# Kernel tuning notes

Hardware: AMD Instinct MI355X
Metric: run time of the kernel (lower is better)

The kernel has to match this reference:

```python
import jax, jax.numpy as jnp
import numpy as np

B, T, N, C = 2, 8, 10242, 64
K, NBR, O = 9, 7, 64


def setup_inputs() -> dict:
    key = jax.random.key(0)
    k1, k2, k3, k4, k5 = jax.random.split(key, 5)
    x = jax.random.normal(k1, (B, T, N, C), dtype=jnp.float32)
    index = jax.random.randint(k2, (N, NBR), 0, N, dtype=jnp.int64)
    itp_mat = jax.random.uniform(k3, (N, NBR, K), dtype=jnp.float32)
    conv_w = jax.random.normal(k4, (O, C, 1, K), dtype=jnp.float32) * (1.0 / np.sqrt(C * K))
    conv_b = jax.random.normal(k5, (O,), dtype=jnp.float32) * 0.01
    return {"x": x, "index": index, "itp_mat": itp_mat, "conv_w": conv_w, "conv_b": conv_b}


def reference(x, index, itp_mat, conv_w, conv_b):
    b, t, n, c = x.shape
    o = conv_w.shape[0]
    # (B,T,N,C) -> (B*T, C, N)
    feats = x.reshape(b * t, n, c).transpose(0, 2, 1)
    # gather neighbors: (BT, C, N, NBR)
    nb = feats[:, :, index]
    # per-node interpolation matmul: (BT, C, N, K)
    itp = jnp.einsum('bcnj,njk->bcnk', nb, itp_mat)
    # Conv2d with kernel (1,K) on width K collapses K fully: (BT, O, N)
    out = jnp.einsum('bcnk,ock->bon', itp, conv_w[:, :, 0, :]) + conv_b[None, :, None]
    # (B, T, O, N) -> (B, T, N, O)
    return out.reshape(b, t, o, n).transpose(0, 1, 3, 2)
```

## Files before the change

kernel.cpp:

```cpp
#include <hip/hip_runtime.h>

#define BT    16
#define NN    10242
#define CC    64
#define KK    9
#define NBR_  7
#define OO    64
#define CK    576
#define MT    16
#define RS    584
#define KT    18

using frag  = __attribute__((ext_vector_type(8))) short;
using f32x4 = __attribute__((ext_vector_type(4))) float;

static __device__ __forceinline__ unsigned short f2bf(float f) {
    union { float f; unsigned u; } v; v.f = f;
    unsigned r = v.u + 0x7fffu + ((v.u >> 16) & 1u);
    return (unsigned short)(r >> 16);
}

static __device__ __forceinline__ unsigned pk2(float a, float b) {
    unsigned r;
    asm("v_cvt_pk_bf16_f32 %0, %1, %2" : "=v"(r) : "v"(a), "v"(b));
    return r;
}

__global__ void pack_w_kernel(const float* __restrict__ w, unsigned short* __restrict__ wb) {
    int i = blockIdx.x * blockDim.x + threadIdx.x;
    if (i >= KT * 4 * 64 * 8) return;
    int j  = i & 7;
    int l  = (i >> 3) & 63;
    int ct = (i >> 9) & 3;
    int t  = i >> 11;
    int q  = t * 32 + (l >> 4) * 8 + j;
    int o  = ct * 16 + (l & 15);
    int c, k;
    if (q < 512) { c = (q & 255) >> 2; k = (q >> 8) * 4 + (q & 3); }
    else         { c = q - 512;        k = 8; }
    wb[i] = f2bf(w[(o * CC + c) * KK + k]);
}

__global__ __launch_bounds__(256, 8) void sphere_conv_kernel(
    const float* __restrict__ x,
    const int*   __restrict__ index,
    const float* __restrict__ m,
    const unsigned short* __restrict__ wb,
    const float* __restrict__ bias,
    float*       __restrict__ out)
{
    __shared__ unsigned short itp_s[MT * RS];

    const int tid  = threadIdx.x;
    const int nt   = blockIdx.x;
    const int bt   = blockIdx.y;
    const int n0   = nt * MT;
    const int w    = tid >> 6;
    const int lane = tid & 63;

    {
        const float* xbt = x + (size_t)bt * NN * CC;

        int nu[4];
        #pragma unroll
        for (int r = 0; r < 4; ++r) {
            const int n = n0 + w * 4 + r;
            nu[r] = __builtin_amdgcn_readfirstlane(n < NN ? n : (NN - 1));
        }

        float xv[4][NBR_];
        #pragma unroll
        for (int r = 0; r < 4; ++r) {
            const int* ip = index + nu[r] * NBR_;
            #pragma unroll
            for (int j = 0; j < NBR_; ++j)
                xv[r][j] = xbt[(size_t)ip[j] * CC + lane];
        }
        __builtin_amdgcn_sched_barrier(0);

        #pragma unroll
        for (int r = 0; r < 4; ++r) {
            const int ns = w * 4 + r;
            const float* mp = m + nu[r] * (NBR_ * KK);
            float acc[KK];
            #pragma unroll
            for (int k = 0; k < KK; ++k) acc[k] = 0.f;
            #pragma unroll
            for (int j = 0; j < NBR_; ++j)
                #pragma unroll
                for (int k = 0; k < KK; ++k)
                    acc[k] = fmaf(xv[r][j], mp[j * KK + k], acc[k]);

            uint2 q0, q1;
            q0.x = pk2(acc[0], acc[1]);
            q0.y = pk2(acc[2], acc[3]);
            q1.x = pk2(acc[4], acc[5]);
            q1.y = pk2(acc[6], acc[7]);
            unsigned short* row = &itp_s[ns * RS];
            *(uint2*)(&row[lane * 4])       = q0;
            *(uint2*)(&row[256 + lane * 4]) = q1;
            row[512 + lane] = f2bf(acc[8]);
        }
    }
    __syncthreads();

    const int ct   = w;
    const int am   = lane & 15;
    const int half = lane >> 4;

    f32x4 acc = (f32x4){0.f, 0.f, 0.f, 0.f};

    const unsigned short* arow = &itp_s[am * RS + half * 8];
    const frag* wbf = (const frag*)wb;

    #pragma unroll
    for (int t = 0; t < KT; ++t) {
        const frag a = *(const frag*)(arow + t * 32);
        const frag b = wbf[(t * 4 + ct) * 64 + lane];
        acc = __builtin_amdgcn_mfma_f32_16x16x32_bf16(a, b, acc, 0, 0, 0);
    }

    const size_t obase = (size_t)bt * NN * OO;
    {
        const int o  = ct * 16 + am;
        const float bo = bias[o];
        #pragma unroll
        for (int i = 0; i < 4; ++i) {
            const int n = n0 + half * 4 + i;
            if (n < NN) out[obase + (size_t)n * OO + o] = acc[i] + bo;
        }
    }
}

extern "C" void kernel_launch(void* const* d_in, const int* in_sizes, int n_in,
                              void* d_out, int out_size, void* d_ws, size_t ws_size,
                              hipStream_t stream) {
    const float* x      = (const float*)d_in[0];
    const int*   index  = (const int*)  d_in[1];
    const float* m      = (const float*)d_in[2];
    const float* conv_w = (const float*)d_in[3];
    const float* conv_b = (const float*)d_in[4];
    float* out = (float*)d_out;
    unsigned short* wb = (unsigned short*)d_ws;

    {
        const int total = KT * 4 * 64 * 8;
        pack_w_kernel<<<(total + 255) / 256, 256, 0, stream>>>(conv_w, wb);
    }
    {
        dim3 grid((NN + MT - 1) / MT, BT);
        sphere_conv_kernel<<<grid, 256, 0, stream>>>(x, index, m, wb, conv_b, out);
    }
}
```

Measured before the change: 145.4 us.

## Warp-specialize producer/consumer waves with double-buffered LDS tiles per block

Turns the one-tile-per-block kernel into a persistent-ish loop over up to 10 tiles per block. Four producer waves gather neighbours and interpolate into one LDS buffer while four consumer waves run the MFMA GEMM and store outputs from the other buffer, with a block barrier between stages. The aim is to overlap gather latency with matrix work and to amortize launch and setup cost. The trade-off is fewer blocks (65x16), 512-thread blocks that need more LDS and registers, and a barrier-bound schedule in which each stage waits for the slower role.

```diff
diff --git a/kernel.cpp b/kernel.cpp
--- a/kernel.cpp
+++ b/kernel.cpp
@@ -1,15 +1,16 @@
 #include <hip/hip_runtime.h>
 
-#define BT    16
-#define NN    10242
-#define CC    64
-#define KK    9
-#define NBR_  7
-#define OO    64
-#define CK    576
-#define MT    16
-#define RS    584
-#define KT    18
+#define BT     16
+#define NN     10242
+#define CC     64
+#define KK     9
+#define NBR_   7
+#define OO     64
+#define MT     16
+#define RS     584
+#define KT     18
+#define NTILES 641
+#define TS     10
 
 using frag  = __attribute__((ext_vector_type(8))) short;
 using f32x4 = __attribute__((ext_vector_type(4))) float;
@@ -41,7 +42,73 @@
     wb[i] = f2bf(w[(o * CC + c) * KK + k]);
 }
 
-__global__ __launch_bounds__(256, 8) void sphere_conv_kernel(
+static __device__ __forceinline__ void produce_tile(
+    const float* __restrict__ xbt, const int* __restrict__ index,
+    const float* __restrict__ m, unsigned short* __restrict__ buf,
+    int n0, int p, int lane)
+{
+    int nu[4];
+    #pragma unroll
+    for (int r = 0; r < 4; ++r) {
+        const int n = n0 + p * 4 + r;
+        nu[r] = __builtin_amdgcn_readfirstlane(n < NN ? n : (NN - 1));
+    }
+    float xv[4][NBR_];
+    #pragma unroll
+    for (int r = 0; r < 4; ++r) {
+        const int* ip = index + nu[r] * NBR_;
+        #pragma unroll
+        for (int j = 0; j < NBR_; ++j)
+            xv[r][j] = xbt[(size_t)ip[j] * CC + lane];
+    }
+    #pragma unroll
+    for (int r = 0; r < 4; ++r) {
+        const int ns = p * 4 + r;
+        const float* mp = m + nu[r] * (NBR_ * KK);
+        float acc[KK];
+        #pragma unroll
+        for (int k = 0; k < KK; ++k) acc[k] = 0.f;
+        #pragma unroll
+        for (int j = 0; j < NBR_; ++j)
+            #pragma unroll
+            for (int k = 0; k < KK; ++k)
+                acc[k] = fmaf(xv[r][j], mp[j * KK + k], acc[k]);
+
+        uint2 q0, q1;
+        q0.x = pk2(acc[0], acc[1]);
+        q0.y = pk2(acc[2], acc[3]);
+        q1.x = pk2(acc[4], acc[5]);
+        q1.y = pk2(acc[6], acc[7]);
+        unsigned short* row = &buf[ns * RS];
+        *(uint2*)(&row[lane * 4])       = q0;
+        *(uint2*)(&row[256 + lane * 4]) = q1;
+        row[512 + lane] = f2bf(acc[8]);
+    }
+}
+
+static __device__ __forceinline__ void consume_tile(
+    const unsigned short* __restrict__ buf, const frag* __restrict__ wbf,
+    float* __restrict__ out, size_t obase, int n0, int ct, int lane, float bo)
+{
+    const int am   = lane & 15;
+    const int half = lane >> 4;
+    const int o    = ct * 16 + am;
+    const unsigned short* arow = &buf[am * RS + half * 8];
+    f32x4 acc = (f32x4){0.f, 0.f, 0.f, 0.f};
+    #pragma unroll
+    for (int t = 0; t < KT; ++t) {
+        const frag a = *(const frag*)(arow + t * 32);
+        const frag b = wbf[(t * 4 + ct) * 64 + lane];
+        acc = __builtin_amdgcn_mfma_f32_16x16x32_bf16(a, b, acc, 0, 0, 0);
+    }
+    #pragma unroll
+    for (int i = 0; i < 4; ++i) {
+        const int n = n0 + half * 4 + i;
+        if (n < NN) out[obase + (size_t)n * OO + o] = acc[i] + bo;
+    }
+}
+
+__global__ __launch_bounds__(512, 8) void sphere_conv_kernel(
     const float* __restrict__ x,
     const int*   __restrict__ index,
     const float* __restrict__ m,
@@ -49,86 +116,33 @@
     const float* __restrict__ bias,
     float*       __restrict__ out)
 {
-    __shared__ unsigned short itp_s[MT * RS];
+    __shared__ unsigned short itp_s[2][MT * RS];
 
-    const int tid  = threadIdx.x;
-    const int nt   = blockIdx.x;
-    const int bt   = blockIdx.y;
-    const int n0   = nt * MT;
-    const int w    = tid >> 6;
-    const int lane = tid & 63;
+    const int tid    = threadIdx.x;
+    const int w      = tid >> 6;
+    const int lane   = tid & 63;
+    const int bt     = blockIdx.y;
+    const int nt0    = blockIdx.x * TS;
+    const int ntiles = (NTILES - nt0) < TS ? (NTILES - nt0) : TS;
 
-    {
-        const float* xbt = x + (size_t)bt * NN * CC;
+    const float* xbt   = x + (size_t)bt * NN * CC;
+    const size_t obase = (size_t)bt * NN * OO;
+    const frag*  wbf   = (const frag*)wb;
 
-        int nu[4];
-        #pragma unroll
-        for (int r = 0; r < 4; ++r) {
-            const int n = n0 + w * 4 + r;
-            nu[r] = __builtin_amdgcn_readfirstlane(n < NN ? n : (NN - 1));
+    const bool isprod = (w < 4);
+    const int  role   = isprod ? w : (w - 4);
+    const float bo    = bias[(isprod ? 0 : role * 16) + (lane & 15)];
+
+    for (int s = 0; s <= ntiles; ++s) {
+        if (isprod) {
+            if (s < ntiles)
+                produce_tile(xbt, index, m, itp_s[s & 1], (nt0 + s) * MT, role, lane);
+        } else {
+            if (s >= 1)
+                consume_tile(itp_s[(s - 1) & 1], wbf, out, obase,
+                             (nt0 + s - 1) * MT, role, lane, bo);
         }
-
-        float xv[4][NBR_];
-        #pragma unroll
-        for (int r = 0; r < 4; ++r) {
-            const int* ip = index + nu[r] * NBR_;
-            #pragma unroll
-            for (int j = 0; j < NBR_; ++j)
-                xv[r][j] = xbt[(size_t)ip[j] * CC + lane];
-        }
-        __builtin_amdgcn_sched_barrier(0);
-
-        #pragma unroll
-        for (int r = 0; r < 4; ++r) {
-            const int ns = w * 4 + r;
-            const float* mp = m + nu[r] * (NBR_ * KK);
-            float acc[KK];
-            #pragma unroll
-            for (int k = 0; k < KK; ++k) acc[k] = 0.f;
-            #pragma unroll
-            for (int j = 0; j < NBR_; ++j)
-                #pragma unroll
-                for (int k = 0; k < KK; ++k)
-                    acc[k] = fmaf(xv[r][j], mp[j * KK + k], acc[k]);
-
-            uint2 q0, q1;
-            q0.x = pk2(acc[0], acc[1]);
-            q0.y = pk2(acc[2], acc[3]);
-            q1.x = pk2(acc[4], acc[5]);
-            q1.y = pk2(acc[6], acc[7]);
-            unsigned short* row = &itp_s[ns * RS];
-            *(uint2*)(&row[lane * 4])       = q0;
-            *(uint2*)(&row[256 + lane * 4]) = q1;
-            row[512 + lane] = f2bf(acc[8]);
-        }
-    }
-    __syncthreads();
-
-    const int ct   = w;
-    const int am   = lane & 15;
-    const int half = lane >> 4;
-
-    f32x4 acc = (f32x4){0.f, 0.f, 0.f, 0.f};
-
-    const unsigned short* arow = &itp_s[am * RS + half * 8];
-    const frag* wbf = (const frag*)wb;
-
-    #pragma unroll
-    for (int t = 0; t < KT; ++t) {
-        const frag a = *(const frag*)(arow + t * 32);
-        const frag b = wbf[(t * 4 + ct) * 64 + lane];
-        acc = __builtin_amdgcn_mfma_f32_16x16x32_bf16(a, b, acc, 0, 0, 0);
-    }
-
-    const size_t obase = (size_t)bt * NN * OO;
-    {
-        const int o  = ct * 16 + am;
-        const float bo = bias[o];
-        #pragma unroll
-        for (int i = 0; i < 4; ++i) {
-            const int n = n0 + half * 4 + i;
-            if (n < NN) out[obase + (size_t)n * OO + o] = acc[i] + bo;
-        }
+        __syncthreads();
     }
 }
 
@@ -148,7 +162,7 @@
         pack_w_kernel<<<(total + 255) / 256, 256, 0, stream>>>(conv_w, wb);
     }
     {
-        dim3 grid((NN + MT - 1) / MT, BT);
-        sphere_conv_kernel<<<grid, 256, 0, stream>>>(x, index, m, wb, conv_b, out);
+        dim3 grid((NTILES + TS - 1) / TS, BT);
+        sphere_conv_kernel<<<grid, 512, 0, stream>>>(x, index, m, wb, conv_b, out);
     }
 }
```

Measured after the change: 187.9 us. 1.29x slower.

## Stage neighbor gathers into LDS via global_load_lds 16-byte DMA

Applied to the files above, without the earlier changes.

Replaces the per-lane 4-byte gathers of neighbor feature rows with global_load_lds 16-byte transfers that write straight into a per-wave LDS staging area. Each wave loads its 28 neighbor rows as seven DMA instructions. The interpolation then reads from LDS, and the bf16 results are written into the shared tile after a barrier, because that tile now aliases the staging buffer. Shared memory grows to 28KB and the occupancy hint drops from 8 to 5 blocks. The trade is fewer, wider memory instructions against lower occupancy and an extra barrier.

```diff
diff --git a/kernel.cpp b/kernel.cpp
--- a/kernel.cpp
+++ b/kernel.cpp
@@ -6,10 +6,10 @@
 #define KK    9
 #define NBR_  7
 #define OO    64
-#define CK    576
 #define MT    16
 #define RS    584
 #define KT    18
+#define STG   7168
 
 using frag  = __attribute__((ext_vector_type(8))) short;
 using f32x4 = __attribute__((ext_vector_type(4))) float;
@@ -41,7 +41,7 @@
     wb[i] = f2bf(w[(o * CC + c) * KK + k]);
 }
 
-__global__ __launch_bounds__(256, 8) void sphere_conv_kernel(
+__global__ __launch_bounds__(256, 5) void sphere_conv_kernel(
     const float* __restrict__ x,
     const int*   __restrict__ index,
     const float* __restrict__ m,
@@ -49,7 +49,8 @@
     const float* __restrict__ bias,
     float*       __restrict__ out)
 {
-    __shared__ unsigned short itp_s[MT * RS];
+    __shared__ __align__(16) unsigned char smem[4 * STG];
+    unsigned short* itp_s = (unsigned short*)smem;
 
     const int tid  = threadIdx.x;
     const int nt   = blockIdx.x;
@@ -57,58 +58,87 @@
     const int n0   = nt * MT;
     const int w    = tid >> 6;
     const int lane = tid & 63;
+    const int sel  = lane >> 4;
+    const int lo16 = lane & 15;
+
+    int nu[4];
+    #pragma unroll
+    for (int r = 0; r < 4; ++r) {
+        const int n = n0 + w * 4 + r;
+        nu[r] = __builtin_amdgcn_readfirstlane(n < NN ? n : (NN - 1));
+    }
+    int ids[4 * NBR_];
+    #pragma unroll
+    for (int r = 0; r < 4; ++r) {
+        const int* ip = index + nu[r] * NBR_;
+        #pragma unroll
+        for (int j = 0; j < NBR_; ++j) ids[r * NBR_ + j] = ip[j];
+    }
 
     {
-        const float* xbt = x + (size_t)bt * NN * CC;
+        const char* xb = (const char*)(x + (size_t)bt * NN * CC);
+        #pragma unroll
+        for (int i = 0; i < 7; ++i) {
+            const int q = i * 4;
+            const int idj = sel == 0 ? ids[q]     : sel == 1 ? ids[q + 1]
+                          : sel == 2 ? ids[q + 2] :            ids[q + 3];
+            const void* src = xb + (size_t)idj * 256 + lo16 * 16;
+            __builtin_amdgcn_global_load_lds(
+                (const __attribute__((address_space(1))) void*)src,
+                (__attribute__((address_space(3))) void*)(smem + w * STG + i * 1024),
+                16, 0, 0);
+        }
+        asm volatile("s_waitcnt vmcnt(0)" ::: "memory");
+    }
 
-        int nu[4];
+    float acc[4][KK];
+    #pragma unroll
+    for (int r = 0; r < 4; ++r)
+        #pragma unroll
+        for (int k = 0; k < KK; ++k) acc[r][k] = 0.f;
+    {
+        const float* xs = (const float*)(smem + w * STG);
         #pragma unroll
         for (int r = 0; r < 4; ++r) {
-            const int n = n0 + w * 4 + r;
-            nu[r] = __builtin_amdgcn_readfirstlane(n < NN ? n : (NN - 1));
-        }
-
-        float xv[4][NBR_];
-        #pragma unroll
-        for (int r = 0; r < 4; ++r) {
-            const int* ip = index + nu[r] * NBR_;
+            const float* mp = m + nu[r] * (NBR_ * KK);
             #pragma unroll
-            for (int j = 0; j < NBR_; ++j)
-                xv[r][j] = xbt[(size_t)ip[j] * CC + lane];
-        }
-        __builtin_amdgcn_sched_barrier(0);
-
-        #pragma unroll
-        for (int r = 0; r < 4; ++r) {
-            const int ns = w * 4 + r;
-            const float* mp = m + nu[r] * (NBR_ * KK);
-            float acc[KK];
-            #pragma unroll
-            for (int k = 0; k < KK; ++k) acc[k] = 0.f;
-            #pragma unroll
-            for (int j = 0; j < NBR_; ++j)
+            for (int j = 0; j < NBR_; ++j) {
+                const float xv = xs[(r * NBR_ + j) * 64 + lane];
                 #pragma unroll
                 for (int k = 0; k < KK; ++k)
-                    acc[k] = fmaf(xv[r][j], mp[j * KK + k], acc[k]);
-
-            uint2 q0, q1;
-            q0.x = pk2(acc[0], acc[1]);
-            q0.y = pk2(acc[2], acc[3]);
-            q1.x = pk2(acc[4], acc[5]);
-            q1.y = pk2(acc[6], acc[7]);
-            unsigned short* row = &itp_s[ns * RS];
-            *(uint2*)(&row[lane * 4])       = q0;
-            *(uint2*)(&row[256 + lane * 4]) = q1;
-            row[512 + lane] = f2bf(acc[8]);
+                    acc[r][k] = fmaf(xv, mp[j * KK + k], acc[r][k]);
+            }
         }
     }
+
+    uint2 q0s[4], q1s[4];
+    unsigned short h8[4];
+    #pragma unroll
+    for (int r = 0; r < 4; ++r) {
+        q0s[r].x = pk2(acc[r][0], acc[r][1]);
+        q0s[r].y = pk2(acc[r][2], acc[r][3]);
+        q1s[r].x = pk2(acc[r][4], acc[r][5]);
+        q1s[r].y = pk2(acc[r][6], acc[r][7]);
+        h8[r]    = f2bf(acc[r][8]);
+    }
+
+    __syncthreads();
+
+    #pragma unroll
+    for (int r = 0; r < 4; ++r) {
+        unsigned short* row = &itp_s[(w * 4 + r) * RS];
+        *(uint2*)(&row[lane * 4])       = q0s[r];
+        *(uint2*)(&row[256 + lane * 4]) = q1s[r];
+        row[512 + lane] = h8[r];
+    }
+
     __syncthreads();
 
     const int ct   = w;
     const int am   = lane & 15;
     const int half = lane >> 4;
 
-    f32x4 acc = (f32x4){0.f, 0.f, 0.f, 0.f};
+    f32x4 cacc = (f32x4){0.f, 0.f, 0.f, 0.f};
 
     const unsigned short* arow = &itp_s[am * RS + half * 8];
     const frag* wbf = (const frag*)wb;
@@ -117,7 +147,7 @@
     for (int t = 0; t < KT; ++t) {
         const frag a = *(const frag*)(arow + t * 32);
         const frag b = wbf[(t * 4 + ct) * 64 + lane];
-        acc = __builtin_amdgcn_mfma_f32_16x16x32_bf16(a, b, acc, 0, 0, 0);
+        cacc = __builtin_amdgcn_mfma_f32_16x16x32_bf16(a, b, cacc, 0, 0, 0);
     }
 
     const size_t obase = (size_t)bt * NN * OO;
@@ -127,7 +157,7 @@
         #pragma unroll
         for (int i = 0; i < 4; ++i) {
             const int n = n0 + half * 4 + i;
-            if (n < NN) out[obase + (size_t)n * OO + o] = acc[i] + bo;
+            if (n < NN) out[obase + (size_t)n * OO + o] = cacc[i] + bo;
         }
     }
 }
```

After: 163.3 us. 1.12x slower.

## Double node tile per block and hoist weight fragments into registers

Applied to the files above, without the earlier changes.

Each block now processes 32 nodes instead of 16. Each wave gathers two chunks of four nodes and then runs two MFMA passes that reuse weight fragments preloaded into registers with inline-asm global loads at kernel start. The goal is to halve the weight fragment traffic per node and to overlap the weight loads with the gather phase. In exchange, shared memory doubles to about 37KB, register pressure rises from holding 18 fragments, launch bounds drop to 4 blocks per SM, and the grid halves, which could reduce occupancy and latency hiding.

```diff
diff --git a/kernel.cpp b/kernel.cpp
--- a/kernel.cpp
+++ b/kernel.cpp
@@ -6,8 +6,7 @@
 #define KK    9
 #define NBR_  7
 #define OO    64
-#define CK    576
-#define MT    16
+#define MT    32
 #define RS    584
 #define KT    18
 
@@ -41,7 +40,7 @@
     wb[i] = f2bf(w[(o * CC + c) * KK + k]);
 }
 
-__global__ __launch_bounds__(256, 8) void sphere_conv_kernel(
+__global__ __launch_bounds__(256, 4) void sphere_conv_kernel(
     const float* __restrict__ x,
     const int*   __restrict__ index,
     const float* __restrict__ m,
@@ -58,48 +57,60 @@
     const int w    = tid >> 6;
     const int lane = tid & 63;
 
+    frag bfr[KT];
+    {
+        const unsigned short* wbp = wb;
+        #pragma unroll
+        for (int t = 0; t < KT; ++t) {
+            const unsigned voff = (unsigned)(((t * 4 + w) * 64 + lane) * 16);
+            asm volatile("global_load_dwordx4 %0, %1, %2"
+                         : "=v"(bfr[t]) : "v"(voff), "s"(wbp));
+        }
+    }
+
     {
         const float* xbt = x + (size_t)bt * NN * CC;
+        #pragma unroll
+        for (int rc = 0; rc < 2; ++rc) {
+            int nu[4];
+            #pragma unroll
+            for (int r = 0; r < 4; ++r) {
+                const int n = n0 + w * 8 + rc * 4 + r;
+                nu[r] = __builtin_amdgcn_readfirstlane(n < NN ? n : (NN - 1));
+            }
 
-        int nu[4];
-        #pragma unroll
-        for (int r = 0; r < 4; ++r) {
-            const int n = n0 + w * 4 + r;
-            nu[r] = __builtin_amdgcn_readfirstlane(n < NN ? n : (NN - 1));
-        }
+            float xv[4][NBR_];
+            #pragma unroll
+            for (int r = 0; r < 4; ++r) {
+                const int* ip = index + nu[r] * NBR_;
+                #pragma unroll
+                for (int j = 0; j < NBR_; ++j)
+                    xv[r][j] = xbt[(size_t)ip[j] * CC + lane];
+            }
 
-        float xv[4][NBR_];
-        #pragma unroll
-        for (int r = 0; r < 4; ++r) {
-            const int* ip = index + nu[r] * NBR_;
             #pragma unroll
-            for (int j = 0; j < NBR_; ++j)
-                xv[r][j] = xbt[(size_t)ip[j] * CC + lane];
-        }
-        __builtin_amdgcn_sched_barrier(0);
+            for (int r = 0; r < 4; ++r) {
+                const int ns = w * 8 + rc * 4 + r;
+                const float* mp = m + nu[r] * (NBR_ * KK);
+                float acc[KK];
+                #pragma unroll
+                for (int k = 0; k < KK; ++k) acc[k] = 0.f;
+                #pragma unroll
+                for (int j = 0; j < NBR_; ++j)
+                    #pragma unroll
+                    for (int k = 0; k < KK; ++k)
+                        acc[k] = fmaf(xv[r][j], mp[j * KK + k], acc[k]);
 
-        #pragma unroll
-        for (int r = 0; r < 4; ++r) {
-            const int ns = w * 4 + r;
-            const float* mp = m + nu[r] * (NBR_ * KK);
-            float acc[KK];
-            #pragma unroll
-            for (int k = 0; k < KK; ++k) acc[k] = 0.f;
-            #pragma unroll
-            for (int j = 0; j < NBR_; ++j)
-                #pragma unroll
-                for (int k = 0; k < KK; ++k)
-                    acc[k] = fmaf(xv[r][j], mp[j * KK + k], acc[k]);
-
-            uint2 q0, q1;
-            q0.x = pk2(acc[0], acc[1]);
-            q0.y = pk2(acc[2], acc[3]);
-            q1.x = pk2(acc[4], acc[5]);
-            q1.y = pk2(acc[6], acc[7]);
-            unsigned short* row = &itp_s[ns * RS];
-            *(uint2*)(&row[lane * 4])       = q0;
-            *(uint2*)(&row[256 + lane * 4]) = q1;
-            row[512 + lane] = f2bf(acc[8]);
+                uint2 q0, q1;
+                q0.x = pk2(acc[0], acc[1]);
+                q0.y = pk2(acc[2], acc[3]);
+                q1.x = pk2(acc[4], acc[5]);
+                q1.y = pk2(acc[6], acc[7]);
+                unsigned short* row = &itp_s[ns * RS];
+                *(uint2*)(&row[lane * 4])       = q0;
+                *(uint2*)(&row[256 + lane * 4]) = q1;
+                row[512 + lane] = f2bf(acc[8]);
+            }
         }
     }
     __syncthreads();
@@ -107,27 +118,23 @@
     const int ct   = w;
     const int am   = lane & 15;
     const int half = lane >> 4;
-
-    f32x4 acc = (f32x4){0.f, 0.f, 0.f, 0.f};
-
-    const unsigned short* arow = &itp_s[am * RS + half * 8];
-    const frag* wbf = (const frag*)wb;
+    const int o    = ct * 16 + am;
+    const float bo = bias[o];
+    const size_t obase = (size_t)bt * NN * OO;
 
     #pragma unroll
-    for (int t = 0; t < KT; ++t) {
-        const frag a = *(const frag*)(arow + t * 32);
-        const frag b = wbf[(t * 4 + ct) * 64 + lane];
-        acc = __builtin_amdgcn_mfma_f32_16x16x32_bf16(a, b, acc, 0, 0, 0);
-    }
-
-    const size_t obase = (size_t)bt * NN * OO;
-    {
-        const int o  = ct * 16 + am;
-        const float bo = bias[o];
+    for (int g = 0; g < 2; ++g) {
+        const unsigned short* arow = &itp_s[(g * 16 + am) * RS + half * 8];
+        f32x4 cacc = (f32x4){0.f, 0.f, 0.f, 0.f};
+        #pragma unroll
+        for (int t = 0; t < KT; ++t) {
+            const frag a = *(const frag*)(arow + t * 32);
+            cacc = __builtin_amdgcn_mfma_f32_16x16x32_bf16(a, bfr[t], cacc, 0, 0, 0);
+        }
         #pragma unroll
         for (int i = 0; i < 4; ++i) {
-            const int n = n0 + half * 4 + i;
-            if (n < NN) out[obase + (size_t)n * OO + o] = acc[i] + bo;
+            const int n = n0 + g * 16 + half * 4 + i;
+            if (n < NN) out[obase + (size_t)n * OO + o] = cacc[i] + bo;
         }
     }
 }
```

After: 158.4 us. +8.9%, slower.
